# Kernel tuning notes

Measured on AMD Instinct MI355X. Metric: run time of the kernel, lower is better.

## Reference

```python
import jax, jax.numpy as jnp
import numpy as np

# Subtraction op config (matches init_kwargs)
K = 7        # kernel_size
S = 1        # stride
P = 3        # padding
D = 1        # dilation
PAD_MODE = 1 # 1 -> reflect, 0 -> zero


def setup_inputs() -> dict:
    key = jax.random.key(0)
    x = jax.random.normal(key, (8, 32, 96, 96), dtype=jnp.float32)
    return {"input": x}


def _subtraction(x):
    # x: [n, c, h, w]
    n, c, h, w = x.shape
    out_h = (h + 2 * P - D * (K - 1) - 1) // S + 1
    out_w = (w + 2 * P - D * (K - 1) - 1) // S + 1
    mode = 'reflect' if PAD_MODE == 1 else 'constant'
    xp = jnp.pad(x, ((0, 0), (0, 0), (P, P), (P, P)), mode=mode)
    # center: input sampled with stride S (unfold with kernel=1, no padding)
    center = x[:, :, ::S, ::S][:, :, :out_h, :out_w]  # [n, c, oh, ow]
    # neighbors: dilated k x k window gather from padded input (strided slices,
    # fixed K*K loop -- no large index arrays, no dynamic shapes)
    patches = []
    for i in range(K):
        for j in range(K):
            patches.append(
                xp[:, :,
                   i * D : i * D + (out_h - 1) * S + 1 : S,
                   j * D : j * D + (out_w - 1) * S + 1 : S])
    nb = jnp.stack(patches, axis=2)            # [n, c, K*K, oh, ow]
    out = center[:, :, None, :, :] - nb        # center minus each neighbor
    return out.reshape(n, c, K * K, out_h * out_w)


def reference(input):
    return _subtraction(input)
```

## Files before the change

### kernel.cpp

```cpp
#include <hip/hip_runtime.h>


constexpr int H = 96, W = 96, PP = 3, KS = 7;
constexpr int PLANE = H * W;
constexpr int NF4 = PLANE / 4;
constexpr int W4 = W / 4;

__device__ __forceinline__ int refl(int t) {
    int r = t < 0 ? -t : t;
    return r >= H ? 2 * (H - 1) - r : r;
}

__global__ __launch_bounds__(256) void subtraction_kernel(
    const float* __restrict__ x, float* __restrict__ out) {
    __shared__ float lds[PLANE];

    const int plane = blockIdx.x;
    const int kc    = blockIdx.y;
    const int di    = kc - PP;

    const float* xp = x + (size_t)plane * PLANE;
    for (int i = threadIdx.x; i < NF4; i += 256)
        ((float4*)lds)[i] = ((const float4*)xp)[i];
    __syncthreads();

    float* op = out + (size_t)plane * (KS * KS) * PLANE
                    + (size_t)kc * KS * PLANE;

    #pragma unroll
    for (int kk = 0; kk < KS; ++kk) {
        const int dj = kk - PP;
        float4* o4 = (float4*)(op + (size_t)kk * PLANE);
        for (int f = threadIdx.x; f < NF4; f += 256) {
            const int row = f / W4;
            const int c4  = f - row * W4;
            const int ow0 = c4 * 4;
            const int nr  = refl(row + di);
            const float* nrow = lds + nr * W;
            const float4 c = ((const float4*)lds)[f];
            float4 v;
            v.x = c.x - nrow[refl(ow0 + 0 + dj)];
            v.y = c.y - nrow[refl(ow0 + 1 + dj)];
            v.z = c.z - nrow[refl(ow0 + 2 + dj)];
            v.w = c.w - nrow[refl(ow0 + 3 + dj)];
            o4[f] = v;
        }
    }
}

extern "C" void kernel_launch(void* const* d_in, const int* in_sizes, int n_in,
                              void* d_out, int out_size, void* d_ws, size_t ws_size,
                              hipStream_t stream) {
    const float* x = (const float*)d_in[0];
    float* out = (float*)d_out;
    const int n_planes = in_sizes[0] / PLANE;
    dim3 grid(n_planes, KS);
    subtraction_kernel<<<grid, 256, 0, stream>>>(x, out);
}
```

Before: 461.4 us.

## Pre-pad LDS rows with reflected halo and reuse one neighbor window across all column offsets

The input plane is stored in LDS with a four-float halo on each side of every row, filled with reflected values. This removes per-element reflect arithmetic on columns. Each thread loads the center float4 and a 12-float neighbor window once, then produces all seven column-shifted outputs from registers instead of re-reading LDS per offset. The loop interchange makes each iteration store to seven separate output planes, and the fixed 9-iteration trip count relies on PLANE/4 being 2304.

```diff
diff --git a/kernel.cpp b/kernel.cpp
--- a/kernel.cpp
+++ b/kernel.cpp
@@ -3,8 +3,9 @@
 
 constexpr int H = 96, W = 96, PP = 3, KS = 7;
 constexpr int PLANE = H * W;
-constexpr int NF4 = PLANE / 4;
 constexpr int W4 = W / 4;
+constexpr int NQ = PLANE / 4;
+constexpr int LROW = 104;
 
 __device__ __forceinline__ int refl(int t) {
     int r = t < 0 ? -t : t;
@@ -13,37 +14,52 @@
 
 __global__ __launch_bounds__(256) void subtraction_kernel(
     const float* __restrict__ x, float* __restrict__ out) {
-    __shared__ float lds[PLANE];
+    __shared__ float lds[H * LROW];
 
+    const int tid   = threadIdx.x;
     const int plane = blockIdx.x;
     const int kc    = blockIdx.y;
     const int di    = kc - PP;
 
     const float* xp = x + (size_t)plane * PLANE;
-    for (int i = threadIdx.x; i < NF4; i += 256)
-        ((float4*)lds)[i] = ((const float4*)xp)[i];
+
+    for (int i = tid; i < NQ; i += 256) {
+        const int r = i / W4, c = i - r * W4;
+        *(float4*)(lds + r * LROW + 4 + c * 4) = ((const float4*)xp)[i];
+    }
+    if (tid < H) {
+        const float* g = xp + tid * W;
+        float* pr = lds + tid * LROW;
+        pr[0] = 0.f;     pr[1] = g[3];    pr[2] = g[2];    pr[3] = g[1];
+        pr[100] = g[94]; pr[101] = g[93]; pr[102] = g[92]; pr[103] = 0.f;
+    }
     __syncthreads();
 
-    float* op = out + (size_t)plane * (KS * KS) * PLANE
-                    + (size_t)kc * KS * PLANE;
+    float* op = out + (size_t)plane * (KS * KS) * PLANE + (size_t)kc * KS * PLANE;
 
-    #pragma unroll
-    for (int kk = 0; kk < KS; ++kk) {
-        const int dj = kk - PP;
-        float4* o4 = (float4*)(op + (size_t)kk * PLANE);
-        for (int f = threadIdx.x; f < NF4; f += 256) {
-            const int row = f / W4;
-            const int c4  = f - row * W4;
-            const int ow0 = c4 * 4;
-            const int nr  = refl(row + di);
-            const float* nrow = lds + nr * W;
-            const float4 c = ((const float4*)lds)[f];
+    for (int it = 0; it < 9; ++it) {
+        const int f   = tid + it * 256;
+        const int row = f / W4;
+        const int c4  = f - row * W4;
+        const int nr  = refl(row + di);
+        const float* crow = lds + row * LROW;
+        const float* nrow = lds + nr * LROW;
+        const float4 c  = *(const float4*)(crow + 4 + c4 * 4);
+        const float4 q0 = *(const float4*)(nrow + c4 * 4);
+        const float4 q1 = *(const float4*)(nrow + c4 * 4 + 4);
+        const float4 q2 = *(const float4*)(nrow + c4 * 4 + 8);
+        const float r12[12] = {q0.x, q0.y, q0.z, q0.w,
+                               q1.x, q1.y, q1.z, q1.w,
+                               q2.x, q2.y, q2.z, q2.w};
+        #pragma unroll
+        for (int kk = 0; kk < KS; ++kk) {
+            const int s = kk + 1;
             float4 v;
-            v.x = c.x - nrow[refl(ow0 + 0 + dj)];
-            v.y = c.y - nrow[refl(ow0 + 1 + dj)];
-            v.z = c.z - nrow[refl(ow0 + 2 + dj)];
-            v.w = c.w - nrow[refl(ow0 + 3 + dj)];
-            o4[f] = v;
+            v.x = c.x - r12[s + 0];
+            v.y = c.y - r12[s + 1];
+            v.z = c.z - r12[s + 2];
+            v.w = c.w - r12[s + 3];
+            ((float4*)(op + (size_t)kk * PLANE))[f] = v;
         }
     }
 }
```

After: 457.7 us. About the same (-0.8%).
